# Kernel tuning notes

Measured on AMD Instinct MI355X. Metric: run time of the kernel, lower is better.

Reference implementation:

```python
import jax, jax.numpy as jnp
import numpy as np

GAMMA = 0.1      # L1 weight
N_STEPS = 10     # inner ISTA/RMSProp iterations
RHO = 0.9        # RMSProp decay
LR = 0.001
MOMENTUM = 0.9
EPS = 1e-8       # RMSProp epsilon
ABS_EPS = 1e-6   # smooth-abs epsilon (seya diff_abs)


def setup_inputs() -> dict:
    key = jax.random.key(0)
    k1, k2 = jax.random.split(key)
    B, D_in, D_out = 32768, 128, 512
    inputs = jax.random.normal(k1, (B, D_in), dtype=jnp.float32)
    # glorot_uniform for W of shape (output_dim, input_dim)
    limit = float(np.sqrt(6.0 / (D_out + D_in)))
    W = jax.random.uniform(k2, (D_out, D_in), jnp.float32, -limit, limit)
    return {"inputs": inputs, "W": W}


def _grad_x(x, W, inputs):
    # cost = sum((inputs - x @ W)^2) + gamma * sum(sqrt(x^2 + ABS_EPS))
    recon = x @ W                        # [B, D_in]
    g = 2.0 * ((recon - inputs) @ W.T)   # analytic d(rec_error)/dx, [B, D_out]
    g = g + GAMMA * x / jnp.sqrt(x * x + ABS_EPS)  # d(smooth L1)/dx
    return g


def reference(inputs, W):
    B = inputs.shape[0]
    D_out = W.shape[0]
    x0 = jnp.zeros((B, D_out), inputs.dtype)
    a1_0 = jnp.zeros_like(x0)
    a2_0 = jnp.zeros_like(x0)

    def step(carry, _):
        x, a1, a2 = carry
        g = _grad_x(x, W, inputs)
        new_a1 = RHO * a1 + (1.0 - RHO) * g * g
        upd = LR * g / jnp.sqrt(new_a1 + EPS)
        new_a2 = MOMENTUM * a2 - upd
        new_x = x + MOMENTUM * new_a2 - upd
        return (new_x, new_a1, new_a2), None

    (xT, _, _), _ = jax.lax.scan(step, (x0, a1_0, a2_0), None, length=N_STEPS)
    return xT  # final sparse codes [B, D_out] (return_reconstruction=False)
```

## Files before the change

kernel.cpp:

```cpp
#include <hip/hip_runtime.h>


#define BSZ   32768
#define DIN   128
#define DOUT  512
#define RTILE 16
#define NSTEP 10
#define NT    512
#define NBLOCKS (BSZ / RTILE)

__global__ void sc_pack(const float* __restrict__ W, float* __restrict__ W4,
                        float* __restrict__ Wt4) {
    const int tid = blockIdx.x * blockDim.x + threadIdx.x;
    const int j = tid >> 7;
    const int i = tid & 127;
    const float v = W[j * DIN + i];
    W4 [(j >> 2) * 512  + i * 4 + (j & 3)] = v;
    Wt4[(i >> 2) * 2048 + j * 4 + (i & 3)] = v;
}

__global__ __launch_bounds__(NT, 6)
void sc_fused(const float* __restrict__ inp, const float4* __restrict__ W4,
              const float4* __restrict__ Wt4, float* __restrict__ out)
{
    __shared__ float x_lds[RTILE][DOUT];
    __shared__ float d_lds[RTILE][DIN];

    const int t = threadIdx.x;
    const int row0 = blockIdx.x * RTILE;

    const int i_p1 = t & 127;
    const int rg   = (t >> 7) * 4;
    const int j0   = t;

    float xs[RTILE], a1[RTILE], a2[RTILE];
#pragma unroll
    for (int r = 0; r < RTILE; ++r) { xs[r] = 0.f; a1[r] = 0.f; a2[r] = 0.f; }

    float inr[4];
#pragma unroll
    for (int rr = 0; rr < 4; ++rr)
        inr[rr] = inp[(row0 + rg + rr) * DIN + i_p1];

    const float4* __restrict__ w4p  = W4 + i_p1;
    const float4* __restrict__ wt4p = Wt4 + j0;

    for (int step = 0; step < NSTEP; ++step) {
        if (step == 0) {
#pragma unroll
            for (int rr = 0; rr < 4; ++rr)
                d_lds[rg + rr][i_p1] = 0.0f - inr[rr];
        } else {
            float acc[4];
#pragma unroll
            for (int rr = 0; rr < 4; ++rr) acc[rr] = 0.f;

#pragma unroll 2
            for (int jb = 0; jb < DOUT / 4; ++jb) {
                const float4 wv = w4p[jb * 128];
#pragma unroll
                for (int rr = 0; rr < 4; ++rr) {
                    const float4 xv = *(const float4*)&x_lds[rg + rr][jb * 4];
                    acc[rr] = fmaf(xv.x, wv.x, acc[rr]);
                    acc[rr] = fmaf(xv.y, wv.y, acc[rr]);
                    acc[rr] = fmaf(xv.z, wv.z, acc[rr]);
                    acc[rr] = fmaf(xv.w, wv.w, acc[rr]);
                }
            }
#pragma unroll
            for (int rr = 0; rr < 4; ++rr)
                d_lds[rg + rr][i_p1] = acc[rr] - inr[rr];
        }
        __syncthreads();

        {
            float acc2[RTILE];
#pragma unroll
            for (int r = 0; r < RTILE; ++r) acc2[r] = 0.f;

#pragma unroll 2
            for (int ib = 0; ib < DIN / 4; ++ib) {
                const float4 wq = wt4p[ib * 512];
#pragma unroll
                for (int r = 0; r < RTILE; ++r) {
                    const float4 dv = *(const float4*)&d_lds[r][ib * 4];
                    acc2[r] = fmaf(dv.x, wq.x, acc2[r]);
                    acc2[r] = fmaf(dv.y, wq.y, acc2[r]);
                    acc2[r] = fmaf(dv.z, wq.z, acc2[r]);
                    acc2[r] = fmaf(dv.w, wq.w, acc2[r]);
                }
            }

#pragma unroll
            for (int r = 0; r < RTILE; ++r) {
                const float xv  = xs[r];
                const float g   = 2.f * acc2[r] + 0.1f * xv * rsqrtf(xv * xv + 1e-6f);
                const float na1 = 0.9f * a1[r] + 0.1f * g * g;
                a1[r] = na1;
                const float upd = 0.001f * g * rsqrtf(na1 + 1e-8f);
                const float na2 = 0.9f * a2[r] - upd;
                a2[r] = na2;
                const float xn = xv + 0.9f * na2 - upd;
                xs[r] = xn;
                x_lds[r][j0] = xn;
            }
            __syncthreads();
        }
    }

    for (int k = t; k < RTILE * DOUT; k += NT)
        out[row0 * DOUT + k] = (&x_lds[0][0])[k];
}

extern "C" void kernel_launch(void* const* d_in, const int* in_sizes, int n_in,
                              void* d_out, int out_size, void* d_ws, size_t ws_size,
                              hipStream_t stream) {
    const float* inputs = (const float*)d_in[0];
    const float* W      = (const float*)d_in[1];
    float* out          = (float*)d_out;
    float* W4           = (float*)d_ws;
    float* Wt4          = (float*)d_ws + 65536;

    sc_pack<<<dim3(256), dim3(256), 0, stream>>>(W, W4, Wt4);
    sc_fused<<<dim3(NBLOCKS), dim3(NT), 0, stream>>>(inputs, (const float4*)W4,
                                                     (const float4*)Wt4, out);
}
```

Baseline: 1.974 ms.

## Register-tile both matmul phases per thread and keep codes in LDS

Each thread now computes a 2x2 output tile in the reconstruction matmul and a 4x4 tile in the gradient matmul, replacing the earlier 4x1 and 16x1 shapes. This lowers LDS reads per FMA and lets each LDS vector and weight float4 feed more FMAs. The code x is no longer held in registers; it is read and written as float4 in LDS. Launch bounds drop from 6 to 2 so the wider accumulators fit, which risks lower occupancy and less latency hiding.

```diff
diff --git a/kernel.cpp b/kernel.cpp
--- a/kernel.cpp
+++ b/kernel.cpp
@@ -9,6 +9,8 @@
 #define NT    512
 #define NBLOCKS (BSZ / RTILE)
 
+typedef __attribute__((ext_vector_type(2))) float f32x2;
+
 __global__ void sc_pack(const float* __restrict__ W, float* __restrict__ W4,
                         float* __restrict__ Wt4) {
     const int tid = blockIdx.x * blockDim.x + threadIdx.x;
@@ -19,7 +21,7 @@
     Wt4[(i >> 2) * 2048 + j * 4 + (i & 3)] = v;
 }
 
-__global__ __launch_bounds__(NT, 6)
+__global__ __launch_bounds__(NT, 2)
 void sc_fused(const float* __restrict__ inp, const float4* __restrict__ W4,
               const float4* __restrict__ Wt4, float* __restrict__ out)
 {
@@ -29,87 +31,143 @@
     const int t = threadIdx.x;
     const int row0 = blockIdx.x * RTILE;
 
-    const int i_p1 = t & 127;
-    const int rg   = (t >> 7) * 4;
-    const int j0   = t;
+    const int rg = (t >> 6) * 2;
+    const int ic = (t & 63) * 2;
+    const int rg2 = (t >> 7) * 4;
+    const int jc  = (t & 127) * 4;
 
-    float xs[RTILE], a1[RTILE], a2[RTILE];
+    float a1[4][4], a2[4][4];
 #pragma unroll
-    for (int r = 0; r < RTILE; ++r) { xs[r] = 0.f; a1[r] = 0.f; a2[r] = 0.f; }
+    for (int r = 0; r < 4; ++r)
+#pragma unroll
+        for (int c = 0; c < 4; ++c) { a1[r][c] = 0.f; a2[r][c] = 0.f; }
 
-    float inr[4];
+    f32x2 inr[2];
 #pragma unroll
-    for (int rr = 0; rr < 4; ++rr)
-        inr[rr] = inp[(row0 + rg + rr) * DIN + i_p1];
+    for (int rr = 0; rr < 2; ++rr)
+        inr[rr] = *(const f32x2*)&inp[(row0 + rg + rr) * DIN + ic];
 
-    const float4* __restrict__ w4p  = W4 + i_p1;
-    const float4* __restrict__ wt4p = Wt4 + j0;
+    {
+        float4* xf4 = (float4*)&x_lds[0][0];
+#pragma unroll
+        for (int k = 0; k < 4; ++k) {
+            float4 z; z.x = z.y = z.z = z.w = 0.f;
+            xf4[t + k * NT] = z;
+        }
+    }
+
+    const float4* __restrict__ w4p  = W4 + ic;
+    const float4* __restrict__ wt4p = Wt4 + jc;
 
     for (int step = 0; step < NSTEP; ++step) {
         if (step == 0) {
 #pragma unroll
-            for (int rr = 0; rr < 4; ++rr)
-                d_lds[rg + rr][i_p1] = 0.0f - inr[rr];
+            for (int rr = 0; rr < 2; ++rr) {
+                f32x2 dv; dv.x = 0.0f - inr[rr].x; dv.y = 0.0f - inr[rr].y;
+                *(f32x2*)&d_lds[rg + rr][ic] = dv;
+            }
         } else {
-            float acc[4];
-#pragma unroll
-            for (int rr = 0; rr < 4; ++rr) acc[rr] = 0.f;
+            float acc[2][2];
+            acc[0][0] = acc[0][1] = acc[1][0] = acc[1][1] = 0.f;
 
 #pragma unroll 2
             for (int jb = 0; jb < DOUT / 4; ++jb) {
-                const float4 wv = w4p[jb * 128];
-#pragma unroll
-                for (int rr = 0; rr < 4; ++rr) {
-                    const float4 xv = *(const float4*)&x_lds[rg + rr][jb * 4];
-                    acc[rr] = fmaf(xv.x, wv.x, acc[rr]);
-                    acc[rr] = fmaf(xv.y, wv.y, acc[rr]);
-                    acc[rr] = fmaf(xv.z, wv.z, acc[rr]);
-                    acc[rr] = fmaf(xv.w, wv.w, acc[rr]);
-                }
+                const float4 wa = w4p[jb * 128];
+                const float4 wb = w4p[jb * 128 + 1];
+                const float4 x0 = *(const float4*)&x_lds[rg + 0][jb * 4];
+                const float4 x1 = *(const float4*)&x_lds[rg + 1][jb * 4];
+                acc[0][0] = fmaf(x0.x, wa.x, acc[0][0]);
+                acc[0][0] = fmaf(x0.y, wa.y, acc[0][0]);
+                acc[0][0] = fmaf(x0.z, wa.z, acc[0][0]);
+                acc[0][0] = fmaf(x0.w, wa.w, acc[0][0]);
+                acc[0][1] = fmaf(x0.x, wb.x, acc[0][1]);
+                acc[0][1] = fmaf(x0.y, wb.y, acc[0][1]);
+                acc[0][1] = fmaf(x0.z, wb.z, acc[0][1]);
+                acc[0][1] = fmaf(x0.w, wb.w, acc[0][1]);
+                acc[1][0] = fmaf(x1.x, wa.x, acc[1][0]);
+                acc[1][0] = fmaf(x1.y, wa.y, acc[1][0]);
+                acc[1][0] = fmaf(x1.z, wa.z, acc[1][0]);
+                acc[1][0] = fmaf(x1.w, wa.w, acc[1][0]);
+                acc[1][1] = fmaf(x1.x, wb.x, acc[1][1]);
+                acc[1][1] = fmaf(x1.y, wb.y, acc[1][1]);
+                acc[1][1] = fmaf(x1.z, wb.z, acc[1][1]);
+                acc[1][1] = fmaf(x1.w, wb.w, acc[1][1]);
             }
 #pragma unroll
-            for (int rr = 0; rr < 4; ++rr)
-                d_lds[rg + rr][i_p1] = acc[rr] - inr[rr];
+            for (int rr = 0; rr < 2; ++rr) {
+                f32x2 dv;
+                dv.x = acc[rr][0] - inr[rr].x;
+                dv.y = acc[rr][1] - inr[rr].y;
+                *(f32x2*)&d_lds[rg + rr][ic] = dv;
+            }
         }
         __syncthreads();
 
         {
-            float acc2[RTILE];
+            float acc2[4][4];
 #pragma unroll
-            for (int r = 0; r < RTILE; ++r) acc2[r] = 0.f;
+            for (int r = 0; r < 4; ++r)
+#pragma unroll
+                for (int c = 0; c < 4; ++c) acc2[r][c] = 0.f;
 
 #pragma unroll 2
             for (int ib = 0; ib < DIN / 4; ++ib) {
-                const float4 wq = wt4p[ib * 512];
+                const float4 q0 = wt4p[ib * 512 + 0];
+                const float4 q1 = wt4p[ib * 512 + 1];
+                const float4 q2 = wt4p[ib * 512 + 2];
+                const float4 q3 = wt4p[ib * 512 + 3];
 #pragma unroll
-                for (int r = 0; r < RTILE; ++r) {
-                    const float4 dv = *(const float4*)&d_lds[r][ib * 4];
-                    acc2[r] = fmaf(dv.x, wq.x, acc2[r]);
-                    acc2[r] = fmaf(dv.y, wq.y, acc2[r]);
-                    acc2[r] = fmaf(dv.z, wq.z, acc2[r]);
-                    acc2[r] = fmaf(dv.w, wq.w, acc2[r]);
+                for (int rr = 0; rr < 4; ++rr) {
+                    const float4 dv = *(const float4*)&d_lds[rg2 + rr][ib * 4];
+                    acc2[rr][0] = fmaf(dv.x, q0.x, acc2[rr][0]);
+                    acc2[rr][0] = fmaf(dv.y, q0.y, acc2[rr][0]);
+                    acc2[rr][0] = fmaf(dv.z, q0.z, acc2[rr][0]);
+                    acc2[rr][0] = fmaf(dv.w, q0.w, acc2[rr][0]);
+                    acc2[rr][1] = fmaf(dv.x, q1.x, acc2[rr][1]);
+                    acc2[rr][1] = fmaf(dv.y, q1.y, acc2[rr][1]);
+                    acc2[rr][1] = fmaf(dv.z, q1.z, acc2[rr][1]);
+                    acc2[rr][1] = fmaf(dv.w, q1.w, acc2[rr][1]);
+                    acc2[rr][2] = fmaf(dv.x, q2.x, acc2[rr][2]);
+                    acc2[rr][2] = fmaf(dv.y, q2.y, acc2[rr][2]);
+                    acc2[rr][2] = fmaf(dv.z, q2.z, acc2[rr][2]);
+                    acc2[rr][2] = fmaf(dv.w, q2.w, acc2[rr][2]);
+                    acc2[rr][3] = fmaf(dv.x, q3.x, acc2[rr][3]);
+                    acc2[rr][3] = fmaf(dv.y, q3.y, acc2[rr][3]);
+                    acc2[rr][3] = fmaf(dv.z, q3.z, acc2[rr][3]);
+                    acc2[rr][3] = fmaf(dv.w, q3.w, acc2[rr][3]);
                 }
             }
 
 #pragma unroll
-            for (int r = 0; r < RTILE; ++r) {
-                const float xv  = xs[r];
-                const float g   = 2.f * acc2[r] + 0.1f * xv * rsqrtf(xv * xv + 1e-6f);
-                const float na1 = 0.9f * a1[r] + 0.1f * g * g;
-                a1[r] = na1;
-                const float upd = 0.001f * g * rsqrtf(na1 + 1e-8f);
-                const float na2 = 0.9f * a2[r] - upd;
-                a2[r] = na2;
-                const float xn = xv + 0.9f * na2 - upd;
-                xs[r] = xn;
-                x_lds[r][j0] = xn;
+            for (int rr = 0; rr < 4; ++rr) {
+                float4 xv = *(const float4*)&x_lds[rg2 + rr][jc];
+                float xn[4];
+#pragma unroll
+                for (int c = 0; c < 4; ++c) {
+                    const float xs  = (c == 0) ? xv.x : (c == 1) ? xv.y
+                                    : (c == 2) ? xv.z : xv.w;
+                    const float g   = 2.f * acc2[rr][c] + 0.1f * xs * rsqrtf(xs * xs + 1e-6f);
+                    const float na1 = 0.9f * a1[rr][c] + 0.1f * g * g;
+                    a1[rr][c] = na1;
+                    const float upd = 0.001f * g * rsqrtf(na1 + 1e-8f);
+                    const float na2 = 0.9f * a2[rr][c] - upd;
+                    a2[rr][c] = na2;
+                    xn[c] = xs + 0.9f * na2 - upd;
+                }
+                float4 xo; xo.x = xn[0]; xo.y = xn[1]; xo.z = xn[2]; xo.w = xn[3];
+                *(float4*)&x_lds[rg2 + rr][jc] = xo;
             }
             __syncthreads();
         }
     }
 
-    for (int k = t; k < RTILE * DOUT; k += NT)
-        out[row0 * DOUT + k] = (&x_lds[0][0])[k];
+    {
+        const float4* xf4 = (const float4*)&x_lds[0][0];
+        float4* of4 = (float4*)(out + row0 * DOUT);
+#pragma unroll
+        for (int k = 0; k < 4; ++k)
+            of4[t + k * NT] = xf4[t + k * NT];
+    }
 }
 
 extern "C" void kernel_launch(void* const* d_in, const int* in_sizes, int n_in,
```

After: 2.174 ms. 10.2% more time.
